# Performance work log

Measured on AMD Instinct MI355X. Metric: run time of the kernel, lower is better.

Reference implementation:

```python
import jax, jax.numpy as jnp
import numpy as np

N_NODES = 50000
N_EDGES = 500000
D = 128
BN_EPS = 1e-5
AGG_EPS = 1e-6


def _batch_norm(x, gamma, beta):
    # training-mode BatchNorm1d: normalize over the batch (row) axis with biased variance
    mean = jnp.mean(x, axis=0)
    var = jnp.var(x, axis=0)
    return (x - mean) * jax.lax.rsqrt(var + BN_EPS) * gamma + beta


def setup_inputs() -> dict:
    key = jax.random.key(0)
    ks = jax.random.split(key, 10)
    w_scale = 1.0 / np.sqrt(D)
    inp = {
        "h": jax.random.normal(ks[0], (N_NODES, D), dtype=jnp.float32),
        "e": jax.random.normal(ks[1], (N_EDGES, D), dtype=jnp.float32),
        "src": jax.random.randint(ks[2], (N_EDGES,), 0, N_NODES),
        "dst": jax.random.randint(ks[3], (N_EDGES,), 0, N_NODES),
    }
    for i, name in enumerate(["A", "B", "C", "D", "E"]):
        inp[f"W_{name}"] = jax.random.normal(ks[4 + i], (D, D), dtype=jnp.float32) * w_scale
        inp[f"b_{name}"] = jnp.zeros((D,), dtype=jnp.float32)
    inp["gamma_h"] = jnp.ones((D,), dtype=jnp.float32)
    inp["beta_h"] = jnp.zeros((D,), dtype=jnp.float32)
    inp["gamma_e"] = jnp.ones((D,), dtype=jnp.float32)
    inp["beta_e"] = jnp.zeros((D,), dtype=jnp.float32)
    return inp


def reference(h, e, src, dst, W_A, b_A, W_B, b_B, W_C, b_C, W_D, b_D, W_E, b_E,
              gamma_h, beta_h, gamma_e, beta_e):
    n = h.shape[0]
    # node projections
    Ah = h @ W_A.T + b_A
    Bh = h @ W_B.T + b_B
    Dh = h @ W_D.T + b_D
    Eh = h @ W_E.T + b_E
    Ce = e @ W_C.T + b_C
    # edge update: u_add_v(Dh, Eh) + Ce
    e_new = Dh[src] + Eh[dst] + Ce            # [E, D]
    sigma = jax.nn.sigmoid(e_new)              # [E, D]
    # gated aggregation to destination nodes
    sum_sigma_h = jax.ops.segment_sum(Bh[src] * sigma, dst, num_segments=n)
    sum_sigma = jax.ops.segment_sum(sigma, dst, num_segments=n)
    h_new = Ah + sum_sigma_h / (sum_sigma + AGG_EPS)
    # batch norm (training-mode) + relu + residual; dropout p=0.0 -> identity
    h_out = jax.nn.relu(_batch_norm(h_new, gamma_h, beta_h))
    e_out = jax.nn.relu(_batch_norm(e_new, gamma_e, beta_e))
    h_out = h + h_out
    e_out = e + e_out
    return h_out, e_out
```

## Files before the change

kernel.cpp:

```cpp
#include <hip/hip_runtime.h>
#include <hip/hip_bf16.h>


#define NN 50000
#define NE 500000
#define DD 128

typedef __attribute__((ext_vector_type(8))) short short8;
typedef __attribute__((ext_vector_type(4))) float floatx4;

__device__ inline short f2bf(float f) {
    unsigned u = __builtin_bit_cast(unsigned, f);
    u += 0x7FFFu + ((u >> 16) & 1u);
    return (short)(u >> 16);
}

__device__ inline short8 load_frag(const float* __restrict__ p) {
    float4 a = *(const float4*)p;
    float4 b = *(const float4*)(p + 4);
    short8 r;
    r[0] = f2bf(a.x); r[1] = f2bf(a.y); r[2] = f2bf(a.z); r[3] = f2bf(a.w);
    r[4] = f2bf(b.x); r[5] = f2bf(b.y); r[6] = f2bf(b.z); r[7] = f2bf(b.w);
    return r;
}

__launch_bounds__(256)
__global__ void node_gemm(const float* __restrict__ h,
                          const float* W0, const float* W1, const float* W2, const float* W3,
                          const float* b0, const float* b1, const float* b2, const float* b3,
                          float* o0, float* o1, float* o2, float* o3) {
    int mtx = blockIdx.y;
    const float* W = (mtx == 0) ? W0 : (mtx == 1) ? W1 : (mtx == 2) ? W2 : W3;
    const float* bias_p = (mtx == 0) ? b0 : (mtx == 1) ? b1 : (mtx == 2) ? b2 : b3;
    float* out = (mtx == 0) ? o0 : (mtx == 1) ? o1 : (mtx == 2) ? o2 : o3;

    int lane = threadIdx.x & 63;
    int wid = threadIdx.x >> 6;
    int m = lane & 15, quad = lane >> 4;
    int gw = blockIdx.x * 4 + wid;
    int nw = gridDim.x * 4;

    short8 wf[8][4];
    float bias[8];
#pragma unroll
    for (int tn = 0; tn < 8; tn++) {
        bias[tn] = bias_p[tn * 16 + m];
#pragma unroll
        for (int c = 0; c < 4; c++)
            wf[tn][c] = load_frag(W + (size_t)(tn * 16 + m) * DD + c * 32 + quad * 8);
    }

    const int NT = NN / 16;
    for (int t = gw; t < NT; t += nw) {
        int rowb = t * 16;
        short8 af[4];
#pragma unroll
        for (int c = 0; c < 4; c++)
            af[c] = load_frag(h + (size_t)(rowb + m) * DD + c * 32 + quad * 8);
        floatx4 acc[8];
#pragma unroll
        for (int tn = 0; tn < 8; tn++) acc[tn] = (floatx4)0.0f;
#pragma unroll
        for (int tn = 0; tn < 8; tn++)
#pragma unroll
            for (int c = 0; c < 4; c++)
                acc[tn] = __builtin_amdgcn_mfma_f32_16x16x32_bf16(af[c], wf[tn][c], acc[tn], 0, 0, 0);
        int r0 = rowb + quad * 4;
#pragma unroll
        for (int r = 0; r < 4; r++) {
            float* op = out + (size_t)(r0 + r) * DD;
#pragma unroll
            for (int tn = 0; tn < 8; tn++) {
                int col = tn * 16 + m;
                op[col] = acc[tn][r] + bias[tn];
            }
        }
    }
}

__launch_bounds__(256)
__global__ void edge_gemm(const float* __restrict__ e,
                          const float* __restrict__ Wc, const float* __restrict__ bc,
                          const float* __restrict__ Dh, const float* __restrict__ Eh,
                          const int* __restrict__ src, const int* __restrict__ dst,
                          float* __restrict__ enew,
                          float* __restrict__ cs_e, float* __restrict__ cq_e) {
    int lane = threadIdx.x & 63;
    int wid = threadIdx.x >> 6;
    int m = lane & 15, quad = lane >> 4;
    int gw = blockIdx.x * 4 + wid;
    int nw = gridDim.x * 4;

    short8 wf[8][4];
    float bias[8];
#pragma unroll
    for (int tn = 0; tn < 8; tn++) {
        bias[tn] = bc[tn * 16 + m];
#pragma unroll
        for (int c = 0; c < 4; c++)
            wf[tn][c] = load_frag(Wc + (size_t)(tn * 16 + m) * DD + c * 32 + quad * 8);
    }

    float ssum[8] = {};
    float ssq[8] = {};

    const int NT = NE / 16;
    for (int t = gw; t < NT; t += nw) {
        int rowb = t * 16;
        short8 af[4];
#pragma unroll
        for (int c = 0; c < 4; c++)
            af[c] = load_frag(e + (size_t)(rowb + m) * DD + c * 32 + quad * 8);
        floatx4 acc[8];
#pragma unroll
        for (int tn = 0; tn < 8; tn++) acc[tn] = (floatx4)0.0f;
#pragma unroll
        for (int tn = 0; tn < 8; tn++)
#pragma unroll
            for (int c = 0; c < 4; c++)
                acc[tn] = __builtin_amdgcn_mfma_f32_16x16x32_bf16(af[c], wf[tn][c], acc[tn], 0, 0, 0);

        int e0 = rowb + quad * 4;
        int4 s4 = *(const int4*)(src + e0);
        int4 d4 = *(const int4*)(dst + e0);
        int sarr[4] = {s4.x, s4.y, s4.z, s4.w};
        int darr[4] = {d4.x, d4.y, d4.z, d4.w};
#pragma unroll
        for (int r = 0; r < 4; r++) {
            const float* dp = Dh + (size_t)sarr[r] * DD;
            const float* ep = Eh + (size_t)darr[r] * DD;
            float* op = enew + (size_t)(e0 + r) * DD;
#pragma unroll
            for (int tn = 0; tn < 8; tn++) {
                int col = tn * 16 + m;
                float v = acc[tn][r] + bias[tn] + dp[col] + ep[col];
                op[col] = v;
                ssum[tn] += v;
                ssq[tn] += v * v;
            }
        }
    }

#pragma unroll
    for (int tn = 0; tn < 8; tn++) {
        float s = ssum[tn], q = ssq[tn];
        s += __shfl_xor(s, 32); s += __shfl_xor(s, 16);
        q += __shfl_xor(q, 32); q += __shfl_xor(q, 16);
        if (quad == 0) {
            atomicAdd(&cs_e[tn * 16 + m], s);
            atomicAdd(&cq_e[tn * 16 + m], q);
        }
    }
}

__global__ void hist_kernel(const int* __restrict__ dst, int* __restrict__ counts) {
    int i = blockIdx.x * blockDim.x + threadIdx.x;
    if (i < NE) atomicAdd(&counts[dst[i]], 1);
}

__global__ void scan_kernel(const int* __restrict__ counts,
                            int* __restrict__ rowptr, int* __restrict__ cursor) {
    __shared__ int lds[1024];
    int t = threadIdx.x;
    const int CH = (NN + 1023) / 1024;
    int begin = t * CH;
    int end = begin + CH; if (end > NN) end = NN; if (begin > NN) begin = NN;
    int s = 0;
    for (int i = begin; i < end; i++) s += counts[i];
    lds[t] = s;
    __syncthreads();
    for (int off = 1; off < 1024; off <<= 1) {
        int v = lds[t];
        int add = (t >= off) ? lds[t - off] : 0;
        __syncthreads();
        lds[t] = v + add;
        __syncthreads();
    }
    int run = (t == 0) ? 0 : lds[t - 1];
    for (int i = begin; i < end; i++) {
        rowptr[i] = run; cursor[i] = run;
        run += counts[i];
    }
    if (t == 1023) rowptr[NN] = run;
}

__global__ void scatter_kernel(const int* __restrict__ src, const int* __restrict__ dst,
                               int* __restrict__ cursor,
                               int* __restrict__ eidx, int* __restrict__ ssrc) {
    int i = blockIdx.x * blockDim.x + threadIdx.x;
    if (i < NE) {
        int d = dst[i];
        int pos = atomicAdd(&cursor[d], 1);
        eidx[pos] = i;
        ssrc[pos] = src[i];
    }
}

__global__ void aggregate(const int* __restrict__ rowptr, const int* __restrict__ eidx,
                          const int* __restrict__ ssrc,
                          const float* __restrict__ enew, const float* __restrict__ Bh,
                          const float* __restrict__ Ah, float* __restrict__ hnew) {
    int v = blockIdx.x;
    int d = threadIdx.x;
    int s = rowptr[v], e = rowptr[v + 1];
    float a1 = 0.f, a2 = 0.f;
    int eid_n = 0, sr_n = 0;
    if (s < e) { eid_n = eidx[s]; sr_n = ssrc[s]; }
    for (int j = s; j < e; j++) {
        int eid = eid_n, sr = sr_n;
        if (j + 1 < e) { eid_n = eidx[j + 1]; sr_n = ssrc[j + 1]; }
        float x = enew[(size_t)eid * DD + d];
        float sig = 1.f / (1.f + __expf(-x));
        a1 = fmaf(sig, Bh[(size_t)sr * DD + d], a1);
        a2 += sig;
    }
    hnew[(size_t)v * DD + d] = Ah[(size_t)v * DD + d] + a1 / (a2 + 1e-6f);
}

__global__ void hstats(const float* __restrict__ hnew, float* __restrict__ cs, float* __restrict__ cq) {
    int d = threadIdx.x;
    float s = 0.f, q = 0.f;
    for (int v = blockIdx.x; v < NN; v += gridDim.x) {
        float x = hnew[(size_t)v * DD + d];
        s += x; q += x * x;
    }
    atomicAdd(&cs[d], s);
    atomicAdd(&cq[d], q);
}

__global__ void finalize(const float* cs_e, const float* cq_e,
                         const float* cs_h, const float* cq_h,
                         const float* ge, const float* be,
                         const float* gh, const float* bh,
                         float* mul_e, float* add_e, float* mul_h, float* add_h) {
    int d = threadIdx.x;
    float me = cs_e[d] / (float)NE;
    float ve = cq_e[d] / (float)NE - me * me;
    float se = rsqrtf(ve + 1e-5f) * ge[d];
    mul_e[d] = se; add_e[d] = be[d] - me * se;
    float mh = cs_h[d] / (float)NN;
    float vh = cq_h[d] / (float)NN - mh * mh;
    float sh = rsqrtf(vh + 1e-5f) * gh[d];
    mul_h[d] = sh; add_h[d] = bh[d] - mh * sh;
}

__global__ void out_transform(float* __restrict__ x, const float* __restrict__ orig,
                              const float* __restrict__ mul, const float* __restrict__ add,
                              int total4) {
    int i = blockIdx.x * blockDim.x + threadIdx.x;
    if (i >= total4) return;
    float4 xv = ((const float4*)x)[i];
    float4 ov = ((const float4*)orig)[i];
    int col = (i * 4) & (DD - 1);
    float4 mu = *(const float4*)(mul + col);
    float4 ad = *(const float4*)(add + col);
    float4 y;
    y.x = fmaxf(fmaf(xv.x, mu.x, ad.x), 0.f) + ov.x;
    y.y = fmaxf(fmaf(xv.y, mu.y, ad.y), 0.f) + ov.y;
    y.z = fmaxf(fmaf(xv.z, mu.z, ad.z), 0.f) + ov.z;
    y.w = fmaxf(fmaf(xv.w, mu.w, ad.w), 0.f) + ov.w;
    ((float4*)x)[i] = y;
}

extern "C" void kernel_launch(void* const* d_in, const int* in_sizes, int n_in,
                              void* d_out, int out_size, void* d_ws, size_t ws_size,
                              hipStream_t stream) {
    const float* h   = (const float*)d_in[0];
    const float* e   = (const float*)d_in[1];
    const int*   src = (const int*)d_in[2];
    const int*   dst = (const int*)d_in[3];
    const float* W_A = (const float*)d_in[4];  const float* b_A = (const float*)d_in[5];
    const float* W_B = (const float*)d_in[6];  const float* b_B = (const float*)d_in[7];
    const float* W_C = (const float*)d_in[8];  const float* b_C = (const float*)d_in[9];
    const float* W_D = (const float*)d_in[10]; const float* b_D = (const float*)d_in[11];
    const float* W_E = (const float*)d_in[12]; const float* b_E = (const float*)d_in[13];
    const float* gamma_h = (const float*)d_in[14]; const float* beta_h = (const float*)d_in[15];
    const float* gamma_e = (const float*)d_in[16]; const float* beta_e = (const float*)d_in[17];

    float* out_h = (float*)d_out;
    float* out_e = out_h + (size_t)NN * DD;

    char* ws = (char*)d_ws;
    float* Ah = (float*)(ws + 0);
    float* Bh = (float*)(ws + 25600000);
    float* Dh = (float*)(ws + 51200000);
    float* Eh = (float*)(ws + 76800000);
    int* rowptr = (int*)(ws + 102400000);
    int* counts = (int*)(ws + 102600192);
    int* cursor = (int*)(ws + 102800192);
    int* eidx   = (int*)(ws + 103000192);
    int* ssrc   = (int*)(ws + 105000192);
    float* stats = (float*)(ws + 107000192);
    float* cs_e = stats + 0 * DD;
    float* cq_e = stats + 1 * DD;
    float* cs_h = stats + 2 * DD;
    float* cq_h = stats + 3 * DD;
    float* mul_e = stats + 4 * DD;
    float* add_e = stats + 5 * DD;
    float* mul_h = stats + 6 * DD;
    float* add_h = stats + 7 * DD;

    hipMemsetAsync(counts, 0, NN * sizeof(int), stream);
    hipMemsetAsync(stats, 0, 4 * DD * sizeof(float), stream);

    node_gemm<<<dim3(128, 4), 256, 0, stream>>>(h, W_A, W_B, W_D, W_E,
                                                b_A, b_B, b_D, b_E,
                                                Ah, Bh, Dh, Eh);

    int nb_edge = (NE + 255) / 256;
    hist_kernel<<<nb_edge, 256, 0, stream>>>(dst, counts);
    scan_kernel<<<1, 1024, 0, stream>>>(counts, rowptr, cursor);
    scatter_kernel<<<nb_edge, 256, 0, stream>>>(src, dst, cursor, eidx, ssrc);

    edge_gemm<<<512, 256, 0, stream>>>(e, W_C, b_C, Dh, Eh, src, dst,
                                       out_e, cs_e, cq_e);

    aggregate<<<NN, DD, 0, stream>>>(rowptr, eidx, ssrc, out_e, Bh, Ah, out_h);

    hstats<<<256, DD, 0, stream>>>(out_h, cs_h, cq_h);

    finalize<<<1, DD, 0, stream>>>(cs_e, cq_e, cs_h, cq_h,
                                   gamma_e, beta_e, gamma_h, beta_h,
                                   mul_e, add_e, mul_h, add_h);

    out_transform<<<(NN * DD / 4 + 255) / 256, 256, 0, stream>>>(out_h, h, mul_h, add_h, NN * DD / 4);
    out_transform<<<(NE * DD / 4 + 255) / 256, 256, 0, stream>>>(out_e, e, mul_e, add_e, NE * DD / 4);
}
```

Before: 1.219 ms.

## Stage GEMM weights in LDS, raise occupancy, and use wave-per-node aggregation

Both GEMM kernels now convert the 128x128 weight matrix to bf16 once into a swizzled LDS buffer instead of holding all 32 fragments in registers. This frees VGPRs, allowing launch bounds of 4 blocks per CU and doubled grid sizes. The bias is folded into the accumulator init. The aggregate kernel switches from a 128-thread block per node to one 64-lane wave per node using float2 loads, which cuts per-block overhead. The cost is extra LDS reads inside the MFMA loop and a bank-conflict risk.

```diff
diff --git a/kernel.cpp b/kernel.cpp
--- a/kernel.cpp
+++ b/kernel.cpp
@@ -24,15 +24,36 @@
     return r;
 }
 
-__launch_bounds__(256)
+__device__ inline void stage_W(const float* __restrict__ W, short* Wlds) {
+    int t = threadIdx.x;
+    int r = t >> 1;
+    int half = t & 1;
+#pragma unroll
+    for (int k = 0; k < 8; k++) {
+        int sub = half * 8 + k;
+        const float* p = W + (size_t)r * DD + sub * 8;
+        float4 a = *(const float4*)p;
+        float4 b = *(const float4*)(p + 4);
+        short8 v;
+        v[0] = f2bf(a.x); v[1] = f2bf(a.y); v[2] = f2bf(a.z); v[3] = f2bf(a.w);
+        v[4] = f2bf(b.x); v[5] = f2bf(b.y); v[6] = f2bf(b.z); v[7] = f2bf(b.w);
+        int slot = r * 16 + (sub ^ (r & 15));
+        *(short8*)&Wlds[slot * 8] = v;
+    }
+}
+
+__launch_bounds__(256, 4)
 __global__ void node_gemm(const float* __restrict__ h,
                           const float* W0, const float* W1, const float* W2, const float* W3,
                           const float* b0, const float* b1, const float* b2, const float* b3,
                           float* o0, float* o1, float* o2, float* o3) {
+    __shared__ short Wlds[DD * DD];
     int mtx = blockIdx.y;
     const float* W = (mtx == 0) ? W0 : (mtx == 1) ? W1 : (mtx == 2) ? W2 : W3;
     const float* bias_p = (mtx == 0) ? b0 : (mtx == 1) ? b1 : (mtx == 2) ? b2 : b3;
     float* out = (mtx == 0) ? o0 : (mtx == 1) ? o1 : (mtx == 2) ? o2 : o3;
+
+    stage_W(W, Wlds);
 
     int lane = threadIdx.x & 63;
     int wid = threadIdx.x >> 6;
@@ -40,15 +61,16 @@
     int gw = blockIdx.x * 4 + wid;
     int nw = gridDim.x * 4;
 
-    short8 wf[8][4];
     float bias[8];
 #pragma unroll
-    for (int tn = 0; tn < 8; tn++) {
-        bias[tn] = bias_p[tn * 16 + m];
-#pragma unroll
-        for (int c = 0; c < 4; c++)
-            wf[tn][c] = load_frag(W + (size_t)(tn * 16 + m) * DD + c * 32 + quad * 8);
-    }
+    for (int tn = 0; tn < 8; tn++) bias[tn] = bias_p[tn * 16 + m];
+
+    int wbase[4];
+#pragma unroll
+    for (int c = 0; c < 4; c++)
+        wbase[c] = (m * 16 + ((c * 4 + quad) ^ m)) * 16;
+
+    __syncthreads();
 
     const int NT = NN / 16;
     for (int t = gw; t < NT; t += nw) {
@@ -59,12 +81,15 @@
             af[c] = load_frag(h + (size_t)(rowb + m) * DD + c * 32 + quad * 8);
         floatx4 acc[8];
 #pragma unroll
-        for (int tn = 0; tn < 8; tn++) acc[tn] = (floatx4)0.0f;
-#pragma unroll
-        for (int tn = 0; tn < 8; tn++)
-#pragma unroll
-            for (int c = 0; c < 4; c++)
-                acc[tn] = __builtin_amdgcn_mfma_f32_16x16x32_bf16(af[c], wf[tn][c], acc[tn], 0, 0, 0);
+        for (int tn = 0; tn < 8; tn++) acc[tn] = (floatx4)bias[tn];
+#pragma unroll
+        for (int tn = 0; tn < 8; tn++) {
+#pragma unroll
+            for (int c = 0; c < 4; c++) {
+                short8 wfr = *(const short8*)((const char*)Wlds + (wbase[c] + tn * 4096));
+                acc[tn] = __builtin_amdgcn_mfma_f32_16x16x32_bf16(af[c], wfr, acc[tn], 0, 0, 0);
+            }
+        }
         int r0 = rowb + quad * 4;
 #pragma unroll
         for (int r = 0; r < 4; r++) {
@@ -72,34 +97,38 @@
 #pragma unroll
             for (int tn = 0; tn < 8; tn++) {
                 int col = tn * 16 + m;
-                op[col] = acc[tn][r] + bias[tn];
+                op[col] = acc[tn][r];
             }
         }
     }
 }
 
-__launch_bounds__(256)
+__launch_bounds__(256, 4)
 __global__ void edge_gemm(const float* __restrict__ e,
                           const float* __restrict__ Wc, const float* __restrict__ bc,
                           const float* __restrict__ Dh, const float* __restrict__ Eh,
                           const int* __restrict__ src, const int* __restrict__ dst,
                           float* __restrict__ enew,
                           float* __restrict__ cs_e, float* __restrict__ cq_e) {
+    __shared__ short Wlds[DD * DD];
+    stage_W(Wc, Wlds);
+
     int lane = threadIdx.x & 63;
     int wid = threadIdx.x >> 6;
     int m = lane & 15, quad = lane >> 4;
     int gw = blockIdx.x * 4 + wid;
     int nw = gridDim.x * 4;
 
-    short8 wf[8][4];
     float bias[8];
 #pragma unroll
-    for (int tn = 0; tn < 8; tn++) {
-        bias[tn] = bc[tn * 16 + m];
-#pragma unroll
-        for (int c = 0; c < 4; c++)
-            wf[tn][c] = load_frag(Wc + (size_t)(tn * 16 + m) * DD + c * 32 + quad * 8);
-    }
+    for (int tn = 0; tn < 8; tn++) bias[tn] = bc[tn * 16 + m];
+
+    int wbase[4];
+#pragma unroll
+    for (int c = 0; c < 4; c++)
+        wbase[c] = (m * 16 + ((c * 4 + quad) ^ m)) * 16;
+
+    __syncthreads();
 
     float ssum[8] = {};
     float ssq[8] = {};
@@ -113,12 +142,15 @@
             af[c] = load_frag(e + (size_t)(rowb + m) * DD + c * 32 + quad * 8);
         floatx4 acc[8];
 #pragma unroll
-        for (int tn = 0; tn < 8; tn++) acc[tn] = (floatx4)0.0f;
-#pragma unroll
-        for (int tn = 0; tn < 8; tn++)
-#pragma unroll
-            for (int c = 0; c < 4; c++)
-                acc[tn] = __builtin_amdgcn_mfma_f32_16x16x32_bf16(af[c], wf[tn][c], acc[tn], 0, 0, 0);
+        for (int tn = 0; tn < 8; tn++) acc[tn] = (floatx4)bias[tn];
+#pragma unroll
+        for (int tn = 0; tn < 8; tn++) {
+#pragma unroll
+            for (int c = 0; c < 4; c++) {
+                short8 wfr = *(const short8*)((const char*)Wlds + (wbase[c] + tn * 4096));
+                acc[tn] = __builtin_amdgcn_mfma_f32_16x16x32_bf16(af[c], wfr, acc[tn], 0, 0, 0);
+            }
+        }
 
         int e0 = rowb + quad * 4;
         int4 s4 = *(const int4*)(src + e0);
@@ -133,7 +165,7 @@
 #pragma unroll
             for (int tn = 0; tn < 8; tn++) {
                 int col = tn * 16 + m;
-                float v = acc[tn][r] + bias[tn] + dp[col] + ep[col];
+                float v = acc[tn][r] + dp[col] + ep[col];
                 op[col] = v;
                 ssum[tn] += v;
                 ssq[tn] += v * v;
@@ -196,25 +228,40 @@
     }
 }
 
+__launch_bounds__(256)
 __global__ void aggregate(const int* __restrict__ rowptr, const int* __restrict__ eidx,
                           const int* __restrict__ ssrc,
                           const float* __restrict__ enew, const float* __restrict__ Bh,
                           const float* __restrict__ Ah, float* __restrict__ hnew) {
-    int v = blockIdx.x;
-    int d = threadIdx.x;
-    int s = rowptr[v], e = rowptr[v + 1];
-    float a1 = 0.f, a2 = 0.f;
-    int eid_n = 0, sr_n = 0;
-    if (s < e) { eid_n = eidx[s]; sr_n = ssrc[s]; }
+    int gw = (blockIdx.x * blockDim.x + threadIdx.x) >> 6;
+    int lane = threadIdx.x & 63;
+    if (gw >= NN) return;
+    int s = rowptr[gw], e = rowptr[gw + 1];
+    int c0 = lane * 2;
+    float a1x = 0.f, a1y = 0.f, a2x = 0.f, a2y = 0.f;
+    float2 xv = {0.f, 0.f}, bv = {0.f, 0.f};
+    if (s < e) {
+        int eid = eidx[s], sr = ssrc[s];
+        xv = *(const float2*)(enew + (size_t)eid * DD + c0);
+        bv = *(const float2*)(Bh + (size_t)sr * DD + c0);
+    }
     for (int j = s; j < e; j++) {
-        int eid = eid_n, sr = sr_n;
-        if (j + 1 < e) { eid_n = eidx[j + 1]; sr_n = ssrc[j + 1]; }
-        float x = enew[(size_t)eid * DD + d];
-        float sig = 1.f / (1.f + __expf(-x));
-        a1 = fmaf(sig, Bh[(size_t)sr * DD + d], a1);
-        a2 += sig;
-    }
-    hnew[(size_t)v * DD + d] = Ah[(size_t)v * DD + d] + a1 / (a2 + 1e-6f);
+        float2 x = xv, b = bv;
+        if (j + 1 < e) {
+            int eid2 = eidx[j + 1], sr2 = ssrc[j + 1];
+            xv = *(const float2*)(enew + (size_t)eid2 * DD + c0);
+            bv = *(const float2*)(Bh + (size_t)sr2 * DD + c0);
+        }
+        float sx = 1.f / (1.f + __expf(-x.x));
+        float sy = 1.f / (1.f + __expf(-x.y));
+        a1x = fmaf(sx, b.x, a1x); a1y = fmaf(sy, b.y, a1y);
+        a2x += sx; a2y += sy;
+    }
+    float2 ah = *(const float2*)(Ah + (size_t)gw * DD + c0);
+    float2 o;
+    o.x = ah.x + a1x / (a2x + 1e-6f);
+    o.y = ah.y + a1y / (a2y + 1e-6f);
+    *(float2*)(hnew + (size_t)gw * DD + c0) = o;
 }
 
 __global__ void hstats(const float* __restrict__ hnew, float* __restrict__ cs, float* __restrict__ cq) {
@@ -303,7 +350,7 @@
     hipMemsetAsync(counts, 0, NN * sizeof(int), stream);
     hipMemsetAsync(stats, 0, 4 * DD * sizeof(float), stream);
 
-    node_gemm<<<dim3(128, 4), 256, 0, stream>>>(h, W_A, W_B, W_D, W_E,
+    node_gemm<<<dim3(256, 4), 256, 0, stream>>>(h, W_A, W_B, W_D, W_E,
                                                 b_A, b_B, b_D, b_E,
                                                 Ah, Bh, Dh, Eh);
 
@@ -312,10 +359,10 @@
     scan_kernel<<<1, 1024, 0, stream>>>(counts, rowptr, cursor);
     scatter_kernel<<<nb_edge, 256, 0, stream>>>(src, dst, cursor, eidx, ssrc);
 
-    edge_gemm<<<512, 256, 0, stream>>>(e, W_C, b_C, Dh, Eh, src, dst,
-                                       out_e, cs_e, cq_e);
-
-    aggregate<<<NN, DD, 0, stream>>>(rowptr, eidx, ssrc, out_e, Bh, Ah, out_h);
+    edge_gemm<<<1024, 256, 0, stream>>>(e, W_C, b_C, Dh, Eh, src, dst,
+                                        out_e, cs_e, cq_e);
+
+    aggregate<<<(NN * 64 + 255) / 256, 256, 0, stream>>>(rowptr, eidx, ssrc, out_e, Bh, Ah, out_h);
 
     hstats<<<256, DD, 0, stream>>>(out_h, cs_h, cq_h);
 
```

New measurement: 1.344 ms. 10.2% more time.
